# Kernel tuning notes

Measured on AMD Instinct MI355X. Metric: run time of the kernel, lower is better.

## Reference

```python
import jax, jax.numpy as jnp
import numpy as np

B, S, H, E = 2, 2048, 16, 64
INV_SCALE = 8.0  # sqrt(head_dim); forward divides scores by this


def setup_inputs() -> dict:
    key = jax.random.key(0)
    ks = jax.random.split(key, 10)
    return {
        "query": jax.random.normal(ks[0], (B, S, H, E), dtype=jnp.float32),
        "key": jax.random.normal(ks[1], (B, S, H, E), dtype=jnp.float32),
        "value": jax.random.normal(ks[2], (B, S, H, E), dtype=jnp.float32),
        "attn_mask": jax.random.randint(ks[3], (B, S), 0, 2, dtype=jnp.int32),
        "Wq": jax.random.normal(ks[4], (E, E), dtype=jnp.float32) / np.sqrt(E),
        "bq": jax.random.normal(ks[5], (E,), dtype=jnp.float32) * 0.02,
        "Wk": jax.random.normal(ks[6], (E, E), dtype=jnp.float32) / np.sqrt(E),
        "bk": jax.random.normal(ks[7], (E,), dtype=jnp.float32) * 0.02,
        "Wv": jax.random.normal(ks[8], (E, E), dtype=jnp.float32) / np.sqrt(E),
        "bv": jax.random.normal(ks[9], (E,), dtype=jnp.float32) * 0.02,
    }


def reference(query, key, value, attn_mask, Wq, bq, Wk, bk, Wv, bv):
    # Linear projections over the last (embed) dim; torch Linear: x @ W.T + b
    q = jnp.einsum('bshe,fe->bhsf', query, Wq) + bq  # [B,H,S,E] (permute 0,2,1,3 fused)
    k = jnp.einsum('bshe,fe->bhsf', key, Wk) + bk
    v = jnp.einsum('bshe,fe->bhsf', value, Wv) + bv
    scores = jnp.einsum('bhqe,bhke->bhqk', q, k) / INV_SCALE  # [B,H,S,S]
    # mask: positions where attn_mask == 0 get -inf, broadcast over (1,1,k_len)
    masked = attn_mask[:, None, None, :] == 0  # [B,1,1,S]
    scores = jnp.where(masked, -jnp.inf, scores)
    attn = jax.nn.softmax(scores, axis=-1)
    out = jnp.einsum('bhqk,bhke->bqhe', attn, v)  # permute back to [B,S,H,E]
    return out
```

## Files before the change

kernel.cpp:

```cpp
#include <hip/hip_runtime.h>


#define BATCH 2
#define SEQ   2048
#define NH    16
#define DE    64
#define LDOF  68
#define NKT   (SEQ / 64)
#define LOG2E 1.44269504088896340736f
#define CSHIFT 16.0f

using bf16x8   = __attribute__((ext_vector_type(8))) __bf16;
using bf16x4   = __attribute__((ext_vector_type(4))) __bf16;
using bf16x2   = __attribute__((ext_vector_type(2))) __bf16;
using floatx2  = __attribute__((ext_vector_type(2))) float;
using floatx4  = __attribute__((ext_vector_type(4))) float;
using floatx16 = __attribute__((ext_vector_type(16))) float;
using ushortx4 = __attribute__((ext_vector_type(4))) unsigned short;
using ushortx8 = __attribute__((ext_vector_type(8))) unsigned short;
using uintx4   = __attribute__((ext_vector_type(4))) unsigned int;
using intx4    = __attribute__((ext_vector_type(4))) int;

__device__ __forceinline__ ushortx4 cvt4(floatx4 f) {
    bf16x4 h = __builtin_convertvector(f, bf16x4);
    return __builtin_bit_cast(ushortx4, h);
}

__device__ __forceinline__ unsigned int pkbf16(float a, float b) {
    floatx2 f = {a, b};
    return __builtin_bit_cast(unsigned int, __builtin_convertvector(f, bf16x2));
}

__device__ __forceinline__ void pl32swap(unsigned int& x, unsigned int& y) {
    __asm__ volatile("v_permlane32_swap_b32 %0, %1" : "+v"(x), "+v"(y));
}

__global__ __launch_bounds__(256) void proj_kernel(
    const float* __restrict__ xq, const float* __restrict__ xk, const float* __restrict__ xv,
    const float* __restrict__ Wq, const float* __restrict__ bq,
    const float* __restrict__ Wk, const float* __restrict__ bk,
    const float* __restrict__ Wv, const float* __restrict__ bv,
    unsigned short* __restrict__ qb, unsigned short* __restrict__ kb,
    unsigned short* __restrict__ vtb)
{
    __shared__ __align__(16) unsigned short Wb[64 * 72];
    __shared__ __align__(16) unsigned short Xb[8 * 1160];
    __shared__ __align__(16) unsigned short Ob[12288];
    __shared__ float blds[64];

    const int t  = threadIdx.x;
    const int bi = blockIdx.x;
    const int hh = bi & 1;
    const int st = (bi >> 1) & 127;
    const int b  = (bi >> 8) & 1;
    const int p  = bi >> 9;
    const int h0 = hh * 8;
    const int lane = t & 63, w = t >> 6, quad = lane >> 4, l16 = lane & 15;

    const float* x    = (p == 0) ? xq : (p == 1) ? xk : xv;
    const float* W    = (p == 0) ? Wq : (p == 1) ? Wk : Wv;
    const float* bias = (p == 0) ? bq : (p == 1) ? bk : bv;

    #pragma unroll
    for (int i = 0; i < 8; ++i) {
        int idx = i * 256 + t;
        int s = idx >> 7, rem = idx & 127, h = rem >> 4, e4 = (rem & 15) * 4;
        floatx4 xv4 = *(const floatx4*)(x + ((size_t)(b * SEQ + st * 16 + s) * NH + h0 + h) * DE + e4);
        *(ushortx4*)&Xb[h * 1160 + s * 72 + e4] = cvt4(xv4);
    }
    #pragma unroll
    for (int i = 0; i < 4; ++i) {
        int idx = i * 256 + t;
        int row = idx >> 4, c4 = (idx & 15) * 4;
        floatx4 wv4 = *(const floatx4*)(W + row * 64 + c4);
        *(ushortx4*)&Wb[row * 72 + c4] = cvt4(wv4);
    }
    if (t < 64) blds[t] = bias[t];
    __syncthreads();

    if (p < 2) {
        bf16x8 a0 = *(const bf16x8*)&Wb[(w * 16 + l16) * 72 + quad * 8];
        bf16x8 a1 = *(const bf16x8*)&Wb[(w * 16 + l16) * 72 + 32 + quad * 8];
        floatx4 bf4 = *(const floatx4*)&blds[w * 16 + quad * 4];
        const float scale = (p == 0) ? 0.125f * LOG2E : 1.0f;
        #pragma unroll
        for (int h = 0; h < 8; ++h) {
            bf16x8 b0 = *(const bf16x8*)&Xb[h * 1160 + l16 * 72 + quad * 8];
            bf16x8 b1 = *(const bf16x8*)&Xb[h * 1160 + l16 * 72 + 32 + quad * 8];
            floatx4 c = {0.f, 0.f, 0.f, 0.f};
            c = __builtin_amdgcn_mfma_f32_16x16x32_bf16(a0, b0, c, 0, 0, 0);
            c = __builtin_amdgcn_mfma_f32_16x16x32_bf16(a1, b1, c, 0, 0, 0);
            floatx4 v;
            v[0] = (c[0] + bf4[0]) * scale; v[1] = (c[1] + bf4[1]) * scale;
            v[2] = (c[2] + bf4[2]) * scale; v[3] = (c[3] + bf4[3]) * scale;
            *(ushortx4*)&Ob[h * 1160 + l16 * 72 + w * 16 + quad * 4] = cvt4(v);
        }
    } else {
        bf16x8 b0 = *(const bf16x8*)&Wb[(w * 16 + l16) * 72 + quad * 8];
        bf16x8 b1 = *(const bf16x8*)&Wb[(w * 16 + l16) * 72 + 32 + quad * 8];
        const float bw = blds[w * 16 + l16];
        #pragma unroll
        for (int h = 0; h < 8; ++h) {
            bf16x8 a0 = *(const bf16x8*)&Xb[h * 1160 + l16 * 72 + quad * 8];
            bf16x8 a1 = *(const bf16x8*)&Xb[h * 1160 + l16 * 72 + 32 + quad * 8];
            floatx4 c = {0.f, 0.f, 0.f, 0.f};
            c = __builtin_amdgcn_mfma_f32_16x16x32_bf16(a0, b0, c, 0, 0, 0);
            c = __builtin_amdgcn_mfma_f32_16x16x32_bf16(a1, b1, c, 0, 0, 0);
            floatx4 v;
            v[0] = c[0] + bw; v[1] = c[1] + bw; v[2] = c[2] + bw; v[3] = c[3] + bw;
            *(ushortx4*)&Ob[h * 1536 + (w * 16 + l16) * 24 + quad * 4] = cvt4(v);
        }
    }
    __syncthreads();

    if (p < 2) {
        unsigned short* dst = (p == 0) ? qb : kb;
        const int rb  = st >> 1;
        const int sl0 = (st & 1) * 16;
        #pragma unroll
        for (int i = 0; i < 4; ++i) {
            int idx = i * 256 + t;
            int j = idx & 7, s = (idx >> 3) & 15, h = idx >> 7;
            ushortx8 v = *(const ushortx8*)&Ob[h * 1160 + s * 72 + j * 8];
            size_t off = ((size_t)((b * 16 + h0 + h) * 64) + rb) * 2048 + j * 256 + (sl0 + s) * 8;
            *(ushortx8*)(dst + off) = v;
        }
    } else {
        const int kt  = st >> 2;
        const int cb  = (st & 3) * 2;
        #pragma unroll
        for (int i = 0; i < 4; ++i) {
            int idx = i * 256 + t;
            int cl = idx & 1, e = (idx >> 1) & 63, h = idx >> 7;
            ushortx8 v = *(const ushortx8*)&Ob[h * 1536 + e * 24 + cl * 8];
            size_t off = (((size_t)(b * 16 + h0 + h) * 32 + kt) * 8 + cb + cl) * 512 + e * 8;
            *(ushortx8*)(vtb + off) = v;
        }
    }
}

__global__ __launch_bounds__(512, 4) void attn_kernel(
    const unsigned short* __restrict__ qb, const unsigned short* __restrict__ kb,
    const unsigned short* __restrict__ vtb, const int* __restrict__ mask,
    float* __restrict__ out)
{
    __shared__ __align__(16) char smem[36864 + 8192];
    float* Ol = (float*)smem;
    float* Ll = (float*)(smem + 34816);
    float* Ml = (float*)(smem + 36864);

    const int wg  = blockIdx.x;
    const int bh  = ((wg >> 3) >> 4) * 8 + (wg & 7);
    const int qt  = (wg >> 3) & 15;
    const int b   = bh >> 4, h = bh & 15;
    const int q0  = qt * 128;
    const int t   = threadIdx.x;
    const int lane = t & 63, w = t >> 6;
    const int hi = lane >> 5, l31 = lane & 31;
    const int qw = w & 3, kblk = w >> 2;

    {
        intx4 mv = *(const intx4*)(mask + b * SEQ + t * 4);
        Ml[t * 4 + 0] = mv[0] ? -CSHIFT : -1e30f;
        Ml[t * 4 + 1] = mv[1] ? -CSHIFT : -1e30f;
        Ml[t * 4 + 2] = mv[2] ? -CSHIFT : -1e30f;
        Ml[t * 4 + 3] = mv[3] ? -CSHIFT : -1e30f;
    }

    const unsigned short* qp = qb + ((size_t)(bh * 64 + qt * 4 + qw)) * 2048 + hi * 256 + l31 * 8;
    bf16x8 qf[4];
    #pragma unroll
    for (int ks = 0; ks < 4; ++ks)
        qf[ks] = *(const bf16x8*)(qp + ks * 512);

    const unsigned short* kp = kb + ((size_t)(bh * 64 + kblk)) * 2048 + hi * 256 + l31 * 8;
    const unsigned short* vp = vtb + (size_t)bh * 131072 + (kblk * 4 + hi) * 512 + l31 * 8;
    const float* Mb = Ml + kblk * 32 + hi * 4;

    __syncthreads();

    floatx16 o0, o1;
    #pragma unroll
    for (int i = 0; i < 16; ++i) { o0[i] = 0.f; o1[i] = 0.f; }
    float lp = 0.f;

    bf16x8 kf0 = *(const bf16x8*)(kp);
    bf16x8 kf1 = *(const bf16x8*)(kp + 512);
    bf16x8 kf2 = *(const bf16x8*)(kp + 1024);
    bf16x8 kf3 = *(const bf16x8*)(kp + 1536);
    bf16x8 vf00 = *(const bf16x8*)(vp);
    bf16x8 vf01 = *(const bf16x8*)(vp + 256);
    bf16x8 vf10 = *(const bf16x8*)(vp + 1024);
    bf16x8 vf11 = *(const bf16x8*)(vp + 1280);

    for (int kt = 0; kt < NKT; ++kt) {
        const int ktn = (kt + 1) & (NKT - 1);

        const float* Mc = Mb + kt * 64;
        floatx16 sc;
        #pragma unroll
        for (int g = 0; g < 4; ++g) {
            floatx4 mb = *(const floatx4*)(Mc + g * 8);
            sc[4 * g + 0] = mb[0]; sc[4 * g + 1] = mb[1];
            sc[4 * g + 2] = mb[2]; sc[4 * g + 3] = mb[3];
        }
        __builtin_amdgcn_s_setprio(1);
        sc = __builtin_amdgcn_mfma_f32_32x32x16_bf16(kf0, qf[0], sc, 0, 0, 0);
        sc = __builtin_amdgcn_mfma_f32_32x32x16_bf16(kf1, qf[1], sc, 0, 0, 0);
        sc = __builtin_amdgcn_mfma_f32_32x32x16_bf16(kf2, qf[2], sc, 0, 0, 0);
        sc = __builtin_amdgcn_mfma_f32_32x32x16_bf16(kf3, qf[3], sc, 0, 0, 0);
        __builtin_amdgcn_s_setprio(0);

        {
            const unsigned short* kq = kp + ktn * 4096;
            kf0 = *(const bf16x8*)(kq);
            kf1 = *(const bf16x8*)(kq + 512);
            kf2 = *(const bf16x8*)(kq + 1024);
            kf3 = *(const bf16x8*)(kq + 1536);
        }

        #pragma unroll
        for (int r = 0; r < 16; ++r)
            sc[r] = __builtin_amdgcn_exp2f(sc[r]);
        {
            float a0 = sc[0] + sc[1],   a1 = sc[2] + sc[3];
            float a2 = sc[4] + sc[5],   a3 = sc[6] + sc[7];
            float a4 = sc[8] + sc[9],   a5 = sc[10] + sc[11];
            float a6 = sc[12] + sc[13], a7 = sc[14] + sc[15];
            lp += ((a0 + a1) + (a2 + a3)) + ((a4 + a5) + (a6 + a7));
        }

        unsigned int wd0 = pkbf16(sc[0], sc[1]),   wd1 = pkbf16(sc[2], sc[3]);
        unsigned int wd2 = pkbf16(sc[4], sc[5]),   wd3 = pkbf16(sc[6], sc[7]);
        unsigned int wd4 = pkbf16(sc[8], sc[9]),   wd5 = pkbf16(sc[10], sc[11]);
        unsigned int wd6 = pkbf16(sc[12], sc[13]), wd7 = pkbf16(sc[14], sc[15]);
        pl32swap(wd0, wd2); pl32swap(wd1, wd3);
        pl32swap(wd4, wd6); pl32swap(wd5, wd7);
        uintx4 f0v = {wd0, wd1, wd2, wd3};
        uintx4 f1v = {wd4, wd5, wd6, wd7};
        bf16x8 pf0 = __builtin_bit_cast(bf16x8, f0v);
        bf16x8 pf1 = __builtin_bit_cast(bf16x8, f1v);

        __builtin_amdgcn_s_setprio(1);
        o0 = __builtin_amdgcn_mfma_f32_32x32x16_bf16(vf00, pf0, o0, 0, 0, 0);
        o1 = __builtin_amdgcn_mfma_f32_32x32x16_bf16(vf01, pf0, o1, 0, 0, 0);
        o0 = __builtin_amdgcn_mfma_f32_32x32x16_bf16(vf10, pf1, o0, 0, 0, 0);
        o1 = __builtin_amdgcn_mfma_f32_32x32x16_bf16(vf11, pf1, o1, 0, 0, 0);
        __builtin_amdgcn_s_setprio(0);

        {
            const unsigned short* vq = vp + ktn * 4096;
            vf00 = *(const bf16x8*)(vq);
            vf01 = *(const bf16x8*)(vq + 256);
            vf10 = *(const bf16x8*)(vq + 1024);
            vf11 = *(const bf16x8*)(vq + 1280);
        }
    }

    const int qrow = qw * 32 + l31;
    Ll[qrow * 4 + kblk * 2 + hi] = lp;
    if (kblk == 1) {
        #pragma unroll
        for (int g = 0; g < 4; ++g) {
            floatx4 t0 = {o0[4*g+0], o0[4*g+1], o0[4*g+2], o0[4*g+3]};
            *(floatx4*)&Ol[qrow * LDOF + g * 8 + hi * 4] = t0;
            floatx4 t1 = {o1[4*g+0], o1[4*g+1], o1[4*g+2], o1[4*g+3]};
            *(floatx4*)&Ol[qrow * LDOF + 32 + g * 8 + hi * 4] = t1;
        }
    }
    __syncthreads();
    if (kblk == 0) {
        floatx4 lv = *(const floatx4*)&Ll[qrow * 4];
        float invl = __builtin_amdgcn_rcpf(lv[0] + lv[1] + lv[2] + lv[3]);
        #pragma unroll
        for (int g = 0; g < 4; ++g) {
            floatx4 t0 = *(floatx4*)&Ol[qrow * LDOF + g * 8 + hi * 4];
            t0[0] = (t0[0] + o0[4*g+0]) * invl; t0[1] = (t0[1] + o0[4*g+1]) * invl;
            t0[2] = (t0[2] + o0[4*g+2]) * invl; t0[3] = (t0[3] + o0[4*g+3]) * invl;
            *(floatx4*)&Ol[qrow * LDOF + g * 8 + hi * 4] = t0;
            floatx4 t1 = *(floatx4*)&Ol[qrow * LDOF + 32 + g * 8 + hi * 4];
            t1[0] = (t1[0] + o1[4*g+0]) * invl; t1[1] = (t1[1] + o1[4*g+1]) * invl;
            t1[2] = (t1[2] + o1[4*g+2]) * invl; t1[3] = (t1[3] + o1[4*g+3]) * invl;
            *(floatx4*)&Ol[qrow * LDOF + 32 + g * 8 + hi * 4] = t1;
        }
    }
    __syncthreads();
    {
        const int quad = lane >> 4, l16 = lane & 15;
        #pragma unroll
        for (int pass = 0; pass < 4; ++pass) {
            int rl  = w * 16 + pass * 4 + quad;
            int col = l16 * 4;
            floatx4 tv = *(const floatx4*)&Ol[rl * LDOF + col];
            *(floatx4*)(out + (((size_t)b * SEQ + q0 + rl) * NH + h) * DE + col) = tv;
        }
    }
}

extern "C" void kernel_launch(void* const* d_in, const int* in_sizes, int n_in,
                              void* d_out, int out_size, void* d_ws, size_t ws_size,
                              hipStream_t stream) {
    const float* query = (const float*)d_in[0];
    const float* key   = (const float*)d_in[1];
    const float* value = (const float*)d_in[2];
    const int*   mask  = (const int*)d_in[3];
    const float* Wq = (const float*)d_in[4];
    const float* bq = (const float*)d_in[5];
    const float* Wk = (const float*)d_in[6];
    const float* bk = (const float*)d_in[7];
    const float* Wv = (const float*)d_in[8];
    const float* bv = (const float*)d_in[9];

    const size_t tensor_elems = (size_t)BATCH * NH * SEQ * DE;
    unsigned short* qb  = (unsigned short*)d_ws;
    unsigned short* kb  = qb + tensor_elems;
    unsigned short* vtb = kb + tensor_elems;

    proj_kernel<<<dim3(3 * BATCH * 128 * 2), 256, 0, stream>>>(
        query, key, value, Wq, bq, Wk, bk, Wv, bv, qb, kb, vtb);
    attn_kernel<<<dim3(512), 512, 0, stream>>>(
        qb, kb, vtb, mask, (float*)d_out);
}
```

Before: 151.9 us.

## Process two query sub-tiles per wave to reuse K/V fragments

Each wave now handles 64 query rows (two 32-row sub-tiles) instead of 32, so every K and V fragment loaded from global memory feeds twice as many MFMAs. Query tile per workgroup grows to 256, the grid halves to 256 blocks, and LDS for the output staging doubles. Mask values for the next key tile are also prefetched into registers alongside K. Register pressure rises (launch bounds drop to 2 blocks per SM) and 256 blocks may underfill the 256 CUs' occupancy.

```diff
diff --git a/kernel.cpp b/kernel.cpp
--- a/kernel.cpp
+++ b/kernel.cpp
@@ -139,21 +139,21 @@
     }
 }
 
-__global__ __launch_bounds__(512, 4) void attn_kernel(
+__global__ __launch_bounds__(512, 2) void attn_kernel(
     const unsigned short* __restrict__ qb, const unsigned short* __restrict__ kb,
     const unsigned short* __restrict__ vtb, const int* __restrict__ mask,
     float* __restrict__ out)
 {
-    __shared__ __align__(16) char smem[36864 + 8192];
+    __shared__ __align__(16) char smem[69632 + 4096 + 8192];
     float* Ol = (float*)smem;
-    float* Ll = (float*)(smem + 34816);
-    float* Ml = (float*)(smem + 36864);
+    float* Ll = (float*)(smem + 69632);
+    float* Ml = (float*)(smem + 73728);
 
     const int wg  = blockIdx.x;
-    const int bh  = ((wg >> 3) >> 4) * 8 + (wg & 7);
-    const int qt  = (wg >> 3) & 15;
+    const int bh  = ((wg >> 3) >> 3) * 8 + (wg & 7);
+    const int qt  = (wg >> 3) & 7;
     const int b   = bh >> 4, h = bh & 15;
-    const int q0  = qt * 128;
+    const int q0  = qt * 256;
     const int t   = threadIdx.x;
     const int lane = t & 63, w = t >> 6;
     const int hi = lane >> 5, l31 = lane & 31;
@@ -167,22 +167,24 @@
         Ml[t * 4 + 3] = mv[3] ? -CSHIFT : -1e30f;
     }
 
-    const unsigned short* qp = qb + ((size_t)(bh * 64 + qt * 4 + qw)) * 2048 + hi * 256 + l31 * 8;
-    bf16x8 qf[4];
+    const unsigned short* qpa = qb + ((size_t)(bh * 64 + qt * 8 + qw * 2)) * 2048 + hi * 256 + l31 * 8;
+    const unsigned short* kp  = kb + ((size_t)(bh * 64 + kblk)) * 2048 + hi * 256 + l31 * 8;
+    const unsigned short* vp  = vtb + (size_t)bh * 131072 + (kblk * 4 + hi) * 512 + l31 * 8;
+    const float* Mb = Ml + kblk * 32 + hi * 4;
+
+    bf16x8 qfa[4], qfb[4];
     #pragma unroll
-    for (int ks = 0; ks < 4; ++ks)
-        qf[ks] = *(const bf16x8*)(qp + ks * 512);
-
-    const unsigned short* kp = kb + ((size_t)(bh * 64 + kblk)) * 2048 + hi * 256 + l31 * 8;
-    const unsigned short* vp = vtb + (size_t)bh * 131072 + (kblk * 4 + hi) * 512 + l31 * 8;
-    const float* Mb = Ml + kblk * 32 + hi * 4;
-
-    __syncthreads();
-
-    floatx16 o0, o1;
+    for (int ks = 0; ks < 4; ++ks) {
+        qfa[ks] = *(const bf16x8*)(qpa + ks * 512);
+        qfb[ks] = *(const bf16x8*)(qpa + 2048 + ks * 512);
+    }
+
+    __syncthreads();
+
+    floatx16 oa0, oa1, ob0, ob1;
     #pragma unroll
-    for (int i = 0; i < 16; ++i) { o0[i] = 0.f; o1[i] = 0.f; }
-    float lp = 0.f;
+    for (int i = 0; i < 16; ++i) { oa0[i] = 0.f; oa1[i] = 0.f; ob0[i] = 0.f; ob1[i] = 0.f; }
+    float lpa = 0.f, lpb = 0.f;
 
     bf16x8 kf0 = *(const bf16x8*)(kp);
     bf16x8 kf1 = *(const bf16x8*)(kp + 512);
@@ -192,23 +194,31 @@
     bf16x8 vf01 = *(const bf16x8*)(vp + 256);
     bf16x8 vf10 = *(const bf16x8*)(vp + 1024);
     bf16x8 vf11 = *(const bf16x8*)(vp + 1280);
+    floatx4 mb0 = *(const floatx4*)(Mb);
+    floatx4 mb1 = *(const floatx4*)(Mb + 8);
+    floatx4 mb2 = *(const floatx4*)(Mb + 16);
+    floatx4 mb3 = *(const floatx4*)(Mb + 24);
 
     for (int kt = 0; kt < NKT; ++kt) {
         const int ktn = (kt + 1) & (NKT - 1);
 
-        const float* Mc = Mb + kt * 64;
-        floatx16 sc;
-        #pragma unroll
-        for (int g = 0; g < 4; ++g) {
-            floatx4 mb = *(const floatx4*)(Mc + g * 8);
-            sc[4 * g + 0] = mb[0]; sc[4 * g + 1] = mb[1];
-            sc[4 * g + 2] = mb[2]; sc[4 * g + 3] = mb[3];
+        floatx16 sa, sb;
+        #pragma unroll
+        for (int j = 0; j < 4; ++j) {
+            sa[j]      = mb0[j]; sb[j]      = mb0[j];
+            sa[4 + j]  = mb1[j]; sb[4 + j]  = mb1[j];
+            sa[8 + j]  = mb2[j]; sb[8 + j]  = mb2[j];
+            sa[12 + j] = mb3[j]; sb[12 + j] = mb3[j];
         }
         __builtin_amdgcn_s_setprio(1);
-        sc = __builtin_amdgcn_mfma_f32_32x32x16_bf16(kf0, qf[0], sc, 0, 0, 0);
-        sc = __builtin_amdgcn_mfma_f32_32x32x16_bf16(kf1, qf[1], sc, 0, 0, 0);
-        sc = __builtin_amdgcn_mfma_f32_32x32x16_bf16(kf2, qf[2], sc, 0, 0, 0);
-        sc = __builtin_amdgcn_mfma_f32_32x32x16_bf16(kf3, qf[3], sc, 0, 0, 0);
+        sa = __builtin_amdgcn_mfma_f32_32x32x16_bf16(kf0, qfa[0], sa, 0, 0, 0);
+        sa = __builtin_amdgcn_mfma_f32_32x32x16_bf16(kf1, qfa[1], sa, 0, 0, 0);
+        sa = __builtin_amdgcn_mfma_f32_32x32x16_bf16(kf2, qfa[2], sa, 0, 0, 0);
+        sa = __builtin_amdgcn_mfma_f32_32x32x16_bf16(kf3, qfa[3], sa, 0, 0, 0);
+        sb = __builtin_amdgcn_mfma_f32_32x32x16_bf16(kf0, qfb[0], sb, 0, 0, 0);
+        sb = __builtin_amdgcn_mfma_f32_32x32x16_bf16(kf1, qfb[1], sb, 0, 0, 0);
+        sb = __builtin_amdgcn_mfma_f32_32x32x16_bf16(kf2, qfb[2], sb, 0, 0, 0);
+        sb = __builtin_amdgcn_mfma_f32_32x32x16_bf16(kf3, qfb[3], sb, 0, 0, 0);
         __builtin_amdgcn_s_setprio(0);
 
         {
@@ -217,35 +227,60 @@
             kf1 = *(const bf16x8*)(kq + 512);
             kf2 = *(const bf16x8*)(kq + 1024);
             kf3 = *(const bf16x8*)(kq + 1536);
-        }
-
-        #pragma unroll
-        for (int r = 0; r < 16; ++r)
-            sc[r] = __builtin_amdgcn_exp2f(sc[r]);
+            const float* Mn = Mb + ktn * 64;
+            mb0 = *(const floatx4*)(Mn);
+            mb1 = *(const floatx4*)(Mn + 8);
+            mb2 = *(const floatx4*)(Mn + 16);
+            mb3 = *(const floatx4*)(Mn + 24);
+        }
+
+        #pragma unroll
+        for (int r = 0; r < 16; ++r) sa[r] = __builtin_amdgcn_exp2f(sa[r]);
+        #pragma unroll
+        for (int r = 0; r < 16; ++r) sb[r] = __builtin_amdgcn_exp2f(sb[r]);
         {
-            float a0 = sc[0] + sc[1],   a1 = sc[2] + sc[3];
-            float a2 = sc[4] + sc[5],   a3 = sc[6] + sc[7];
-            float a4 = sc[8] + sc[9],   a5 = sc[10] + sc[11];
-            float a6 = sc[12] + sc[13], a7 = sc[14] + sc[15];
-            lp += ((a0 + a1) + (a2 + a3)) + ((a4 + a5) + (a6 + a7));
-        }
-
-        unsigned int wd0 = pkbf16(sc[0], sc[1]),   wd1 = pkbf16(sc[2], sc[3]);
-        unsigned int wd2 = pkbf16(sc[4], sc[5]),   wd3 = pkbf16(sc[6], sc[7]);
-        unsigned int wd4 = pkbf16(sc[8], sc[9]),   wd5 = pkbf16(sc[10], sc[11]);
-        unsigned int wd6 = pkbf16(sc[12], sc[13]), wd7 = pkbf16(sc[14], sc[15]);
-        pl32swap(wd0, wd2); pl32swap(wd1, wd3);
-        pl32swap(wd4, wd6); pl32swap(wd5, wd7);
-        uintx4 f0v = {wd0, wd1, wd2, wd3};
-        uintx4 f1v = {wd4, wd5, wd6, wd7};
-        bf16x8 pf0 = __builtin_bit_cast(bf16x8, f0v);
-        bf16x8 pf1 = __builtin_bit_cast(bf16x8, f1v);
+            float a0 = sa[0] + sa[1],   a1 = sa[2] + sa[3];
+            float a2 = sa[4] + sa[5],   a3 = sa[6] + sa[7];
+            float a4 = sa[8] + sa[9],   a5 = sa[10] + sa[11];
+            float a6 = sa[12] + sa[13], a7 = sa[14] + sa[15];
+            lpa += ((a0 + a1) + (a2 + a3)) + ((a4 + a5) + (a6 + a7));
+            float b0 = sb[0] + sb[1],   b1 = sb[2] + sb[3];
+            float b2 = sb[4] + sb[5],   b3 = sb[6] + sb[7];
+            float b4 = sb[8] + sb[9],   b5 = sb[10] + sb[11];
+            float b6 = sb[12] + sb[13], b7 = sb[14] + sb[15];
+            lpb += ((b0 + b1) + (b2 + b3)) + ((b4 + b5) + (b6 + b7));
+        }
+
+        unsigned int a_w0 = pkbf16(sa[0], sa[1]),   a_w1 = pkbf16(sa[2], sa[3]);
+        unsigned int a_w2 = pkbf16(sa[4], sa[5]),   a_w3 = pkbf16(sa[6], sa[7]);
+        unsigned int a_w4 = pkbf16(sa[8], sa[9]),   a_w5 = pkbf16(sa[10], sa[11]);
+        unsigned int a_w6 = pkbf16(sa[12], sa[13]), a_w7 = pkbf16(sa[14], sa[15]);
+        pl32swap(a_w0, a_w2); pl32swap(a_w1, a_w3);
+        pl32swap(a_w4, a_w6); pl32swap(a_w5, a_w7);
+        uintx4 fa0 = {a_w0, a_w1, a_w2, a_w3};
+        uintx4 fa1 = {a_w4, a_w5, a_w6, a_w7};
+        bf16x8 pf0a = __builtin_bit_cast(bf16x8, fa0);
+        bf16x8 pf1a = __builtin_bit_cast(bf16x8, fa1);
+        unsigned int b_w0 = pkbf16(sb[0], sb[1]),   b_w1 = pkbf16(sb[2], sb[3]);
+        unsigned int b_w2 = pkbf16(sb[4], sb[5]),   b_w3 = pkbf16(sb[6], sb[7]);
+        unsigned int b_w4 = pkbf16(sb[8], sb[9]),   b_w5 = pkbf16(sb[10], sb[11]);
+        unsigned int b_w6 = pkbf16(sb[12], sb[13]), b_w7 = pkbf16(sb[14], sb[15]);
+        pl32swap(b_w0, b_w2); pl32swap(b_w1, b_w3);
+        pl32swap(b_w4, b_w6); pl32swap(b_w5, b_w7);
+        uintx4 fb0 = {b_w0, b_w1, b_w2, b_w3};
+        uintx4 fb1 = {b_w4, b_w5, b_w6, b_w7};
+        bf16x8 pf0b = __builtin_bit_cast(bf16x8, fb0);
+        bf16x8 pf1b = __builtin_bit_cast(bf16x8, fb1);
 
         __builtin_amdgcn_s_setprio(1);
-        o0 = __builtin_amdgcn_mfma_f32_32x32x16_bf16(vf00, pf0, o0, 0, 0, 0);
-        o1 = __builtin_amdgcn_mfma_f32_32x32x16_bf16(vf01, pf0, o1, 0, 0, 0);
-        o0 = __builtin_amdgcn_mfma_f32_32x32x16_bf16(vf10, pf1, o0, 0, 0, 0);
-        o1 = __builtin_amdgcn_mfma_f32_32x32x16_bf16(vf11, pf1, o1, 0, 0, 0);
+        oa0 = __builtin_amdgcn_mfma_f32_32x32x16_bf16(vf00, pf0a, oa0, 0, 0, 0);
+        oa1 = __builtin_amdgcn_mfma_f32_32x32x16_bf16(vf01, pf0a, oa1, 0, 0, 0);
+        oa0 = __builtin_amdgcn_mfma_f32_32x32x16_bf16(vf10, pf1a, oa0, 0, 0, 0);
+        oa1 = __builtin_amdgcn_mfma_f32_32x32x16_bf16(vf11, pf1a, oa1, 0, 0, 0);
+        ob0 = __builtin_amdgcn_mfma_f32_32x32x16_bf16(vf00, pf0b, ob0, 0, 0, 0);
+        ob1 = __builtin_amdgcn_mfma_f32_32x32x16_bf16(vf01, pf0b, ob1, 0, 0, 0);
+        ob0 = __builtin_amdgcn_mfma_f32_32x32x16_bf16(vf10, pf1b, ob0, 0, 0, 0);
+        ob1 = __builtin_amdgcn_mfma_f32_32x32x16_bf16(vf11, pf1b, ob1, 0, 0, 0);
         __builtin_amdgcn_s_setprio(0);
 
         {
@@ -257,39 +292,55 @@
         }
     }
 
-    const int qrow = qw * 32 + l31;
-    Ll[qrow * 4 + kblk * 2 + hi] = lp;
+    const int qa  = qw * 64 + l31;
+    const int qbr = qa + 32;
+    Ll[qa * 4 + kblk * 2 + hi]  = lpa;
+    Ll[qbr * 4 + kblk * 2 + hi] = lpb;
     if (kblk == 1) {
         #pragma unroll
         for (int g = 0; g < 4; ++g) {
-            floatx4 t0 = {o0[4*g+0], o0[4*g+1], o0[4*g+2], o0[4*g+3]};
-            *(floatx4*)&Ol[qrow * LDOF + g * 8 + hi * 4] = t0;
-            floatx4 t1 = {o1[4*g+0], o1[4*g+1], o1[4*g+2], o1[4*g+3]};
-            *(floatx4*)&Ol[qrow * LDOF + 32 + g * 8 + hi * 4] = t1;
+            floatx4 ta0 = {oa0[4*g+0], oa0[4*g+1], oa0[4*g+2], oa0[4*g+3]};
+            *(floatx4*)&Ol[qa * LDOF + g * 8 + hi * 4] = ta0;
+            floatx4 ta1 = {oa1[4*g+0], oa1[4*g+1], oa1[4*g+2], oa1[4*g+3]};
+            *(floatx4*)&Ol[qa * LDOF + 32 + g * 8 + hi * 4] = ta1;
+            floatx4 tb0 = {ob0[4*g+0], ob0[4*g+1], ob0[4*g+2], ob0[4*g+3]};
+            *(floatx4*)&Ol[qbr * LDOF + g * 8 + hi * 4] = tb0;
+            floatx4 tb1 = {ob1[4*g+0], ob1[4*g+1], ob1[4*g+2], ob1[4*g+3]};
+            *(floatx4*)&Ol[qbr * LDOF + 32 + g * 8 + hi * 4] = tb1;
         }
     }
     __syncthreads();
     if (kblk == 0) {
-        floatx4 lv = *(const floatx4*)&Ll[qrow * 4];
-        float invl = __builtin_amdgcn_rcpf(lv[0] + lv[1] + lv[2] + lv[3]);
+        floatx4 lva = *(const floatx4*)&Ll[qa * 4];
+        float invla = __builtin_amdgcn_rcpf(lva[0] + lva[1] + lva[2] + lva[3]);
+        floatx4 lvb = *(const floatx4*)&Ll[qbr * 4];
+        float invlb = __builtin_amdgcn_rcpf(lvb[0] + lvb[1] + lvb[2] + lvb[3]);
         #pragma unroll
         for (int g = 0; g < 4; ++g) {
-            floatx4 t0 = *(floatx4*)&Ol[qrow * LDOF + g * 8 + hi * 4];
-            t0[0] = (t0[0] + o0[4*g+0]) * invl; t0[1] = (t0[1] + o0[4*g+1]) * invl;
-            t0[2] = (t0[2] + o0[4*g+2]) * invl; t0[3] = (t0[3] + o0[4*g+3]) * invl;
-            *(floatx4*)&Ol[qrow * LDOF + g * 8 + hi * 4] = t0;
-            floatx4 t1 = *(floatx4*)&Ol[qrow * LDOF + 32 + g * 8 + hi * 4];
-            t1[0] = (t1[0] + o1[4*g+0]) * invl; t1[1] = (t1[1] + o1[4*g+1]) * invl;
-            t1[2] = (t1[2] + o1[4*g+2]) * invl; t1[3] = (t1[3] + o1[4*g+3]) * invl;
-            *(floatx4*)&Ol[qrow * LDOF + 32 + g * 8 + hi * 4] = t1;
+            floatx4 ta0 = *(floatx4*)&Ol[qa * LDOF + g * 8 + hi * 4];
+            ta0[0] = (ta0[0] + oa0[4*g+0]) * invla; ta0[1] = (ta0[1] + oa0[4*g+1]) * invla;
+            ta0[2] = (ta0[2] + oa0[4*g+2]) * invla; ta0[3] = (ta0[3] + oa0[4*g+3]) * invla;
+            *(floatx4*)&Ol[qa * LDOF + g * 8 + hi * 4] = ta0;
+            floatx4 ta1 = *(floatx4*)&Ol[qa * LDOF + 32 + g * 8 + hi * 4];
+            ta1[0] = (ta1[0] + oa1[4*g+0]) * invla; ta1[1] = (ta1[1] + oa1[4*g+1]) * invla;
+            ta1[2] = (ta1[2] + oa1[4*g+2]) * invla; ta1[3] = (ta1[3] + oa1[4*g+3]) * invla;
+            *(floatx4*)&Ol[qa * LDOF + 32 + g * 8 + hi * 4] = ta1;
+            floatx4 tb0 = *(floatx4*)&Ol[qbr * LDOF + g * 8 + hi * 4];
+            tb0[0] = (tb0[0] + ob0[4*g+0]) * invlb; tb0[1] = (tb0[1] + ob0[4*g+1]) * invlb;
+            tb0[2] = (tb0[2] + ob0[4*g+2]) * invlb; tb0[3] = (tb0[3] + ob0[4*g+3]) * invlb;
+            *(floatx4*)&Ol[qbr * LDOF + g * 8 + hi * 4] = tb0;
+            floatx4 tb1 = *(floatx4*)&Ol[qbr * LDOF + 32 + g * 8 + hi * 4];
+            tb1[0] = (tb1[0] + ob1[4*g+0]) * invlb; tb1[1] = (tb1[1] + ob1[4*g+1]) * invlb;
+            tb1[2] = (tb1[2] + ob1[4*g+2]) * invlb; tb1[3] = (tb1[3] + ob1[4*g+3]) * invlb;
+            *(floatx4*)&Ol[qbr * LDOF + 32 + g * 8 + hi * 4] = tb1;
         }
     }
     __syncthreads();
     {
         const int quad = lane >> 4, l16 = lane & 15;
         #pragma unroll
-        for (int pass = 0; pass < 4; ++pass) {
-            int rl  = w * 16 + pass * 4 + quad;
+        for (int pass = 0; pass < 8; ++pass) {
+            int rl  = w * 32 + pass * 4 + quad;
             int col = l16 * 4;
             floatx4 tv = *(const floatx4*)&Ol[rl * LDOF + col];
             *(floatx4*)(out + (((size_t)b * SEQ + q0 + rl) * NH + h) * DE + col) = tv;
@@ -318,6 +369,6 @@
 
     proj_kernel<<<dim3(3 * BATCH * 128 * 2), 256, 0, stream>>>(
         query, key, value, Wq, bq, Wk, bk, Wv, bv, qb, kb, vtb);
-    attn_kernel<<<dim3(512), 512, 0, stream>>>(
+    attn_kernel<<<dim3(256), 512, 0, stream>>>(
         qb, kb, vtb, mask, (float*)d_out);
 }
```

After: 146.6 us. 3.5% less time.
